# Kernel tuning notes

Hardware: AMD Instinct MI355X
Metric: run time of the kernel (lower is better)

Reference implementation:

```python
import jax, jax.numpy as jnp
import numpy as np

NUM_HEADS = 16

def setup_inputs() -> dict:
    key = jax.random.key(0)
    ks = jax.random.split(key, 7)
    B, Q, K, D = 4, 512, 4096, 1024
    return {
        'query':  jax.random.normal(ks[0], (B, Q, D), dtype=jnp.float32),
        'memory': jax.random.normal(ks[1], (B, K, D), dtype=jnp.float32),
        'bias':   jax.random.normal(ks[2], (B, K), dtype=jnp.float32),
        'Wq': jax.random.normal(ks[3], (D, D), dtype=jnp.float32) * (D ** -0.5),
        'Wk': jax.random.normal(ks[4], (D, D), dtype=jnp.float32) * (D ** -0.5),
        'Wv': jax.random.normal(ks[5], (D, D), dtype=jnp.float32) * (D ** -0.5),
        'Wo': jax.random.normal(ks[6], (D, D), dtype=jnp.float32) * (D ** -0.5),
    }

def reference(query, memory, bias, Wq, Wk, Wv, Wo):
    B, Qn, _ = query.shape
    _, Kn, _ = memory.shape
    H = NUM_HEADS
    E = Wq.shape[1]
    dh = E // H
    scale = dh ** -0.5
    # projections (bias-free linears), split heads: [B, H, len, dh]
    q = (query @ Wq).reshape(B, Qn, H, dh).transpose(0, 2, 1, 3)
    k = (memory @ Wk).reshape(B, Kn, H, dh).transpose(0, 2, 1, 3)
    v = (memory @ Wv).reshape(B, Kn, H, dh).transpose(0, 2, 1, 3)
    scores = jnp.einsum('bhqd,bhkd->bhqk', q, k) * scale
    scores = scores + bias[:, None, None, :]          # additive support bias over K
    weights = jax.nn.softmax(scores, axis=-1)          # dropout p=0.0 -> identity
    out = jnp.einsum('bhqk,bhkd->bhqd', weights, v)
    out = out.transpose(0, 2, 1, 3).reshape(B, Qn, E)
    return out @ Wo
```

## Files before the change

### kernel.cpp

```cpp
#include <hip/hip_runtime.h>

typedef __attribute__((ext_vector_type(8))) short bf16x8;
typedef __attribute__((ext_vector_type(4))) short bf16x4;
typedef __attribute__((ext_vector_type(4))) float f32x4;

#define MFMA32(a,b,c) __builtin_amdgcn_mfma_f32_16x16x32_bf16((a),(b),(c),0,0,0)
#define MFMA16(a,b,c) __builtin_amdgcn_mfma_f32_16x16x16bf16_1k((a),(b),(c),0,0,0)
#define LOG2E 1.44269504f

__device__ __forceinline__ unsigned short f2bf(float f) {
  unsigned int u = __float_as_uint(f);
  u += 0x7fffu + ((u >> 16) & 1u);
  return (unsigned short)(u >> 16);
}

__device__ __forceinline__ void cp16(const void* g, void* l) {
  __builtin_amdgcn_global_load_lds((const __attribute__((address_space(1))) void*)g,
                                   (__attribute__((address_space(3))) void*)l, 16, 0, 0);
}

__global__ void conv_both(const float* __restrict__ q, const float* __restrict__ m,
                          const float* __restrict__ bias,
                          unsigned short* __restrict__ qo, unsigned short* __restrict__ mo,
                          float* __restrict__ bz) {
  int i = blockIdx.x * 256 + threadIdx.x;
  if (i < 524288) {
    float4 v = ((const float4*)q)[i];
    ushort4 o; o.x = f2bf(v.x); o.y = f2bf(v.y); o.z = f2bf(v.z); o.w = f2bf(v.w);
    ((ushort4*)qo)[i] = o;
  } else if (i < 4718592) {
    int j = i - 524288;
    float4 v = ((const float4*)m)[j];
    ushort4 o; o.x = f2bf(v.x); o.y = f2bf(v.y); o.z = f2bf(v.z); o.w = f2bf(v.w);
    ((ushort4*)mo)[j] = o;
  } else {
    int j = i - 4718592;
    float4 v = ((const float4*)bias)[j];
    float4 o;
    o.x = __builtin_fmaf(v.x, LOG2E, -16.f);
    o.y = __builtin_fmaf(v.y, LOG2E, -16.f);
    o.z = __builtin_fmaf(v.z, LOG2E, -16.f);
    o.w = __builtin_fmaf(v.w, LOG2E, -16.f);
    ((float4*)bz)[j] = o;
  }
}

__global__ void transpose4(const float* __restrict__ Wq, const float* __restrict__ Wk,
                           const float* __restrict__ Wv, const float* __restrict__ Wo,
                           unsigned short* __restrict__ dst) {
  __shared__ float t[32][33];
  int z = blockIdx.z;
  const float* W = (z == 0) ? Wq : (z == 1) ? Wk : (z == 2) ? Wv : Wo;
  unsigned short* WT = dst + (size_t)z * 1048576;
  int bx = blockIdx.x * 32, by = blockIdx.y * 32;
  int x = threadIdx.x, y0 = threadIdx.y;
#pragma unroll
  for (int r = 0; r < 4; ++r)
    t[y0 + r * 8][x] = W[(size_t)(by + y0 + r * 8) * 1024 + bx + x];
  __syncthreads();
#pragma unroll
  for (int r = 0; r < 4; ++r)
    WT[(size_t)(bx + y0 + r * 8) * 1024 + by + x] = f2bf(t[x][y0 + r * 8]);
}

__global__ __launch_bounds__(256, 2) void gemm_kv(
    const unsigned short* __restrict__ A,
    const unsigned short* __restrict__ Bk,
    const unsigned short* __restrict__ Bv,
    unsigned short* __restrict__ Kp,
    unsigned short* __restrict__ Vt)
{
  __shared__ __attribute__((aligned(16))) unsigned short lds[16384];
  int w = threadIdx.x >> 6, lane = threadIdx.x & 63;
  int lh = lane & 15, q4 = lane >> 4;
  int id = blockIdx.x;
  int xcd = id & 7, j = id >> 3;
  int tm = (xcd * 16 + (j >> 3)) * 128;
  int tn = (j & 7) * 128;
  int wm = (w & 1) * 64, wn = (w >> 1) * 64;

  int srow = lane >> 2;
  int scol = ((lane & 3) ^ ((lane >> 3) & 3)) << 3;
  int q4s = (q4 ^ ((lh >> 1) & 3)) << 3;

  f32x4 acck[4][4] = {}, accv[4][4] = {};

  for (int k0 = 0; k0 < 1024; k0 += 32) {
#pragma unroll
    for (int i = 0; i < 2; ++i) {
      int c = w * 2 + i;
      int row = c * 16 + srow;
      cp16(A  + (size_t)(tm + row) * 1024 + k0 + scol, lds + c * 512);
      cp16(Bk + (size_t)(tn + row) * 1024 + k0 + scol, lds + 4096 + c * 512);
      cp16(Bv + (size_t)(tn + row) * 1024 + k0 + scol, lds + 8192 + c * 512);
    }
    __syncthreads();
    bf16x8 afr[4], bkf[4], bvf[4];
#pragma unroll
    for (int r = 0; r < 4; ++r)
      afr[r] = *(const bf16x8*)(lds + (wm + r * 16 + lh) * 32 + q4s);
#pragma unroll
    for (int c = 0; c < 4; ++c) {
      bkf[c] = *(const bf16x8*)(lds + 4096 + (wn + c * 16 + lh) * 32 + q4s);
      bvf[c] = *(const bf16x8*)(lds + 8192 + (wn + c * 16 + lh) * 32 + q4s);
    }
#pragma unroll
    for (int r = 0; r < 4; ++r)
#pragma unroll
      for (int c = 0; c < 4; ++c) {
        acck[r][c] = MFMA32(afr[r], bkf[c], acck[r][c]);
        accv[r][c] = MFMA32(afr[r], bvf[c], accv[r][c]);
      }
    __syncthreads();
  }

#pragma unroll
  for (int r = 0; r < 4; ++r)
#pragma unroll
    for (int c = 0; c < 4; ++c) {
      int row = tm + wm + r * 16 + q4 * 4;
      int col = tn + wn + c * 16 + lh;
#pragma unroll
      for (int e = 0; e < 4; ++e)
        Kp[(size_t)(row + e) * 1024 + col] = f2bf(acck[r][c][e]);
    }

#pragma unroll
  for (int r = 0; r < 4; ++r)
#pragma unroll
    for (int c = 0; c < 4; ++c) {
      int row = wm + r * 16 + q4 * 4;
      int col = wn + c * 16 + lh;
      ushort4 v4;
      v4.x = f2bf(accv[r][c][0]); v4.y = f2bf(accv[r][c][1]);
      v4.z = f2bf(accv[r][c][2]); v4.w = f2bf(accv[r][c][3]);
      *(ushort4*)(lds + col * 128 + (row ^ ((col & 15) << 3))) = v4;
    }
  __syncthreads();
#pragma unroll
  for (int pass = 0; pass < 8; ++pass) {
    int col = pass * 16 + (threadIdx.x >> 4);
    int jb = threadIdx.x & 15;
    const unsigned short* src = lds + col * 128 + ((jb ^ (col & 15)) << 3);
    *(int4*)(Vt + (size_t)(tn + col) * 16384 + tm + jb * 8) = *(const int4*)src;
  }
}

__global__ __launch_bounds__(256) void gemm_bt64(
    const unsigned short* __restrict__ A, const unsigned short* __restrict__ B,
    float* __restrict__ Cf, unsigned short* __restrict__ Cb,
    int M, int N, int K, float scale)
{
  __shared__ __attribute__((aligned(16))) unsigned short lds[6144];
  int w = threadIdx.x >> 6, lane = threadIdx.x & 63;
  int lh = lane & 15, q4 = lane >> 4;
  int tm = blockIdx.y * 128, tn = blockIdx.x * 64;
  int wm = (w & 1) * 64, wn = (w >> 1) * 32;

  int srow = lane >> 2;
  int scol = ((lane & 3) ^ ((lane >> 3) & 3)) << 3;
  int q4s = (q4 ^ ((lh >> 1) & 3)) << 3;

  f32x4 acc[4][2] = {};

  for (int k0 = 0; k0 < K; k0 += 32) {
#pragma unroll
    for (int i = 0; i < 2; ++i) {
      int c = w * 2 + i;
      int row = c * 16 + srow;
      cp16(A + (size_t)(tm + row) * K + k0 + scol, lds + c * 512);
    }
    {
      int row = w * 16 + srow;
      cp16(B + (size_t)(tn + row) * K + k0 + scol, lds + 4096 + w * 512);
    }
    __syncthreads();
    bf16x8 afr[4], bfr[2];
#pragma unroll
    for (int r = 0; r < 4; ++r)
      afr[r] = *(const bf16x8*)(lds + (wm + r * 16 + lh) * 32 + q4s);
#pragma unroll
    for (int c = 0; c < 2; ++c)
      bfr[c] = *(const bf16x8*)(lds + 4096 + (wn + c * 16 + lh) * 32 + q4s);
#pragma unroll
    for (int r = 0; r < 4; ++r)
#pragma unroll
      for (int c = 0; c < 2; ++c)
        acc[r][c] = MFMA32(afr[r], bfr[c], acc[r][c]);
    __syncthreads();
  }

#pragma unroll
  for (int r = 0; r < 4; ++r)
#pragma unroll
    for (int c = 0; c < 2; ++c)
#pragma unroll
      for (int e = 0; e < 4; ++e) {
        int row = tm + wm + r * 16 + q4 * 4 + e;
        int col = tn + wn + c * 16 + lh;
        if (Cb) Cb[(size_t)row * N + col] = f2bf(acc[r][c][e] * scale);
        else    Cf[(size_t)row * N + col] = acc[r][c][e] * scale;
      }
}

__global__ __launch_bounds__(256) void attn_kernel(
    const unsigned short* __restrict__ Q, const unsigned short* __restrict__ Kp,
    const unsigned short* __restrict__ VT, const float* __restrict__ bz,
    float* __restrict__ po, float* __restrict__ lp)
{
  __shared__ __attribute__((aligned(16))) unsigned short Klds[4096];
  __shared__ __attribute__((aligned(16))) unsigned short Vlds[4096];
  int w = threadIdx.x >> 6, lane = threadIdx.x & 63;
  int lh = lane & 15, q4 = lane >> 4;

  int id = blockIdx.x;
  int xcd = id & 7, j = id >> 3;
  int ql = j & 7;
  int half = ql & 1, qt = ql >> 1;
  int bh = (j >> 3) * 8 + xcd;
  int b = bh >> 4, h = bh & 15;
  int q0 = qt * 128;
  int t00 = half * 2048;

  const unsigned short* Qb = Q + (size_t)(b * 512 + q0 + w * 32) * 1024 + h * 64;
  const unsigned short* Kb = Kp + (size_t)(b * 4096) * 1024 + h * 64;
  const unsigned short* Vb = VT + (size_t)(h * 64) * 16384 + b * 4096;
  const float* bzg = bz + (size_t)b * 4096;

  bf16x8 bq[2][2];
#pragma unroll
  for (int s = 0; s < 2; ++s)
#pragma unroll
    for (int th = 0; th < 2; ++th)
      bq[s][th] = *(const bf16x8*)(Qb + (size_t)(s * 16 + lh) * 1024 + th * 32 + q4 * 8);

  f32x4 oa[2][4] = {};
  float ls[2] = {0.f, 0.f};

  int rl = lane >> 3, blk = lane & 7;
  int sw = ((blk ^ rl) * 8);

  for (int ti = 0; ti < 32; ++ti) {
    int t = t00 + ti * 64;
#pragma unroll
    for (int r = 0; r < 2; ++r) {
      int seg = r * 4 + w;
      int row = seg * 8 + rl;
      cp16(Kb + (size_t)(t + row) * 1024 + sw, Klds + seg * 512);
      cp16(Vb + (size_t)row * 16384 + t + sw, Vlds + seg * 512);
    }
    __syncthreads();

    float4 bz4[4];
#pragma unroll
    for (int c = 0; c < 4; ++c)
      bz4[c] = *(const float4*)(bzg + t + c * 16 + q4 * 4);

    bf16x8 kf[4][2];
#pragma unroll
    for (int c = 0; c < 4; ++c)
#pragma unroll
      for (int th = 0; th < 2; ++th)
        kf[c][th] = *(const bf16x8*)(Klds + (c * 16 + lh) * 64 + (((th << 2) + q4) ^ (lh & 7)) * 8);
    bf16x4 vf[4][4];
#pragma unroll
    for (int c = 0; c < 4; ++c)
#pragma unroll
      for (int c2 = 0; c2 < 4; ++c2)
        vf[c][c2] = *(const bf16x4*)(Vlds + (c2 * 16 + lh) * 64 +
                                     (((c << 1) + (q4 >> 1)) ^ (lh & 7)) * 8 + (q4 & 1) * 4);

#pragma unroll
    for (int s = 0; s < 2; ++s) {
#pragma unroll
      for (int c = 0; c < 4; ++c) {
        f32x4 z = {};
        z = MFMA32(kf[c][0], bq[s][0], z);
        z = MFMA32(kf[c][1], bq[s][1], z);
        float bzf[4] = {bz4[c].x, bz4[c].y, bz4[c].z, bz4[c].w};
        bf16x4 pb;
        float ps = 0.f;
#pragma unroll
        for (int e = 0; e < 4; ++e) {
          float p = __builtin_amdgcn_exp2f(z[e] + bzf[e]);
          ps += p;
          pb[e] = (short)f2bf(p);
        }
        ls[s] += ps;
#pragma unroll
        for (int c2 = 0; c2 < 4; ++c2)
          oa[s][c2] = MFMA16(vf[c][c2], pb, oa[s][c2]);
      }
    }
    __syncthreads();
  }

#pragma unroll
  for (int s = 0; s < 2; ++s) {
    ls[s] += __shfl_xor(ls[s], 16);
    ls[s] += __shfl_xor(ls[s], 32);
  }

  int sl = bh * 4 + qt;
  float* pslice = po + (size_t)(half * 256 + sl) * 8192;
#pragma unroll
  for (int s = 0; s < 2; ++s) {
    if (q4 == 0) lp[half * 32768 + sl * 128 + w * 32 + s * 16 + lh] = ls[s];
#pragma unroll
    for (int c2 = 0; c2 < 4; ++c2)
#pragma unroll
      for (int e = 0; e < 4; ++e)
        pslice[(c2 * 16 + q4 * 4 + e) * 128 + w * 32 + s * 16 + lh] = oa[s][c2][e];
  }
}

__global__ void norm_kernel(const float* __restrict__ po, const float* __restrict__ lp,
                            unsigned short* __restrict__ ao) {
  int g = blockIdx.x * 256 + threadIdx.x;
  int d8 = (g & 7) * 8;
  int rowid = g >> 3;
  int bh = rowid >> 9, rq = rowid & 511, qt = rq >> 7, qcol = rq & 127;
  int sl = bh * 4 + qt;
  const float* p0 = po + (size_t)sl * 8192;
  const float* p1 = po + (size_t)(256 + sl) * 8192;
  float l = lp[sl * 128 + qcol] + lp[32768 + sl * 128 + qcol];
  float inv = 1.f / l;
  unsigned short o8[8];
#pragma unroll
  for (int k = 0; k < 8; ++k)
    o8[k] = f2bf((p0[(d8 + k) * 128 + qcol] + p1[(d8 + k) * 128 + qcol]) * inv);
  int b = bh >> 4, h = bh & 15;
  unsigned short* dst = ao + (size_t)(b * 512 + qt * 128 + qcol) * 1024 + h * 64 + d8;
  *(ushort4*)dst = *(ushort4*)o8;
  *(ushort4*)(dst + 4) = *(ushort4*)(o8 + 4);
}

extern "C" void kernel_launch(void* const* d_in, const int* in_sizes, int n_in,
                              void* d_out, int out_size, void* d_ws, size_t ws_size,
                              hipStream_t stream) {
  const float* query  = (const float*)d_in[0];
  const float* memory = (const float*)d_in[1];
  const float* bias   = (const float*)d_in[2];
  const float* Wq     = (const float*)d_in[3];
  const float* Wk     = (const float*)d_in[4];
  const float* Wv     = (const float*)d_in[5];
  const float* Wo     = (const float*)d_in[6];
  float* out = (float*)d_out;

  unsigned short* ws  = (unsigned short*)d_ws;
  unsigned short* qbf = ws;
  unsigned short* mbf = qbf + 2097152;
  unsigned short* WqT = mbf + 16777216;
  unsigned short* WkT = WqT + 1048576;
  unsigned short* WvT = WkT + 1048576;
  unsigned short* WoT = WvT + 1048576;
  unsigned short* qp  = WoT + 1048576;
  unsigned short* kp  = qp + 2097152;
  unsigned short* vT  = kp + 16777216;
  unsigned short* ao  = vT + 16777216;
  float* bzw = (float*)(ao + 2097152);
  float* po = (float*)ws;
  float* lp = po + 4194304;

  conv_both<<<18448, 256, 0, stream>>>(query, memory, bias, qbf, mbf, bzw);
  transpose4<<<dim3(32, 32, 4), dim3(32, 8), 0, stream>>>(Wq, Wk, Wv, Wo, WqT);

  gemm_bt64<<<dim3(16, 16), 256, 0, stream>>>(qbf, WqT, nullptr, qp, 2048, 1024, 1024, 0.125f * LOG2E);
  gemm_kv<<<1024, 256, 0, stream>>>(mbf, WkT, WvT, kp, vT);

  attn_kernel<<<512, 256, 0, stream>>>(qp, kp, vT, bzw, po, lp);
  norm_kernel<<<1024, 256, 0, stream>>>(po, lp, ao);

  gemm_bt64<<<dim3(16, 16), 256, 0, stream>>>(ao, WoT, out, nullptr, 2048, 1024, 1024, 1.f);
}
```

Baseline: 303.0 us.

## Restructure KV projection GEMM with 256x128 tiles and double-buffered async pipeline

Rewrites the fused K/V projection GEMM to use 512-thread blocks on 256x128 output tiles with K-step 64, staging A/K/V tiles into a double-buffered 128KB LDS via direct global-to-LDS loads. The main loop is split into four MFMA phases with interleaved prefetches of the next tile, explicit vmcnt waits, raw s_barrier with sched barriers, and setprio around MFMA bursts. This aims to hide global load latency and raise MFMA utilisation. In exchange it uses much more LDS per block, which lowers occupancy, and relies on hand-tuned wait counts that must match the issue order exactly.

```diff
diff --git a/kernel.cpp b/kernel.cpp
--- a/kernel.cpp
+++ b/kernel.cpp
@@ -7,6 +7,10 @@
 #define MFMA32(a,b,c) __builtin_amdgcn_mfma_f32_16x16x32_bf16((a),(b),(c),0,0,0)
 #define MFMA16(a,b,c) __builtin_amdgcn_mfma_f32_16x16x16bf16_1k((a),(b),(c),0,0,0)
 #define LOG2E 1.44269504f
+
+#define BAR() do { asm volatile("s_barrier" ::: "memory"); \
+                   __builtin_amdgcn_sched_barrier(0); } while (0)
+#define VMW(n) asm volatile("s_waitcnt vmcnt(" #n ")" ::: "memory")
 
 __device__ __forceinline__ unsigned short f2bf(float f) {
   unsigned int u = __float_as_uint(f);
@@ -63,85 +67,145 @@
     WT[(size_t)(bx + y0 + r * 8) * 1024 + by + x] = f2bf(t[x][y0 + r * 8]);
 }
 
-__global__ __launch_bounds__(256, 2) void gemm_kv(
+__global__ __launch_bounds__(512, 2) void gemm_kv(
     const unsigned short* __restrict__ A,
     const unsigned short* __restrict__ Bk,
     const unsigned short* __restrict__ Bv,
     unsigned short* __restrict__ Kp,
     unsigned short* __restrict__ Vt)
 {
-  __shared__ __attribute__((aligned(16))) unsigned short lds[16384];
-  int w = threadIdx.x >> 6, lane = threadIdx.x & 63;
-  int lh = lane & 15, q4 = lane >> 4;
-  int id = blockIdx.x;
-  int xcd = id & 7, j = id >> 3;
-  int tm = (xcd * 16 + (j >> 3)) * 128;
-  int tn = (j & 7) * 128;
-  int wm = (w & 1) * 64, wn = (w >> 1) * 64;
-
-  int srow = lane >> 2;
-  int scol = ((lane & 3) ^ ((lane >> 3) & 3)) << 3;
-  int q4s = (q4 ^ ((lh >> 1) & 3)) << 3;
+  __shared__ __attribute__((aligned(16))) unsigned short lds[65536];
+  const int tid = threadIdx.x;
+  const int w = tid >> 6, lane = tid & 63;
+  const int lh = lane & 15, q4 = lane >> 4;
+  const int id = blockIdx.x;
+  const int xcd = id & 7, j = id >> 3;
+  const int tm = (xcd * 8 + (j >> 3)) * 256;
+  const int tn = (j & 7) * 128;
+  const int wm = (w >> 1) * 64, wn = (w & 1) * 64;
+
+  const int r8 = lane >> 3;
+  const int scol = ((lane & 7) ^ r8) * 8;
+  const int srow = w * 8 + r8;
+  const int fs0 = ((0 + q4) ^ (lh & 7)) * 8;
+  const int fs1 = ((4 + q4) ^ (lh & 7)) * 8;
+
+  const unsigned short* Ag = A  + (size_t)tm * 1024 + scol;
+  const unsigned short* Kg = Bk + (size_t)tn * 1024 + scol;
+  const unsigned short* Vg = Bv + (size_t)tn * 1024 + scol;
+
+#define STG_A(BUF,KT,I) cp16(Ag + (size_t)((I)*64 + srow) * 1024 + (KT)*64, \
+                             lds + (BUF)*32768 + (I)*4096 + w*512)
+#define STG_K(BUF,KT,I) cp16(Kg + (size_t)((I)*64 + srow) * 1024 + (KT)*64, \
+                             lds + (BUF)*32768 + 16384 + (I)*4096 + w*512)
+#define STG_V(BUF,KT,I) cp16(Vg + (size_t)((I)*64 + srow) * 1024 + (KT)*64, \
+                             lds + (BUF)*32768 + 24576 + (I)*4096 + w*512)
 
   f32x4 acck[4][4] = {}, accv[4][4] = {};
 
-  for (int k0 = 0; k0 < 1024; k0 += 32) {
-#pragma unroll
-    for (int i = 0; i < 2; ++i) {
-      int c = w * 2 + i;
-      int row = c * 16 + srow;
-      cp16(A  + (size_t)(tm + row) * 1024 + k0 + scol, lds + c * 512);
-      cp16(Bk + (size_t)(tn + row) * 1024 + k0 + scol, lds + 4096 + c * 512);
-      cp16(Bv + (size_t)(tn + row) * 1024 + k0 + scol, lds + 8192 + c * 512);
-    }
-    __syncthreads();
-    bf16x8 afr[4], bkf[4], bvf[4];
-#pragma unroll
-    for (int r = 0; r < 4; ++r)
-      afr[r] = *(const bf16x8*)(lds + (wm + r * 16 + lh) * 32 + q4s);
-#pragma unroll
-    for (int c = 0; c < 4; ++c) {
-      bkf[c] = *(const bf16x8*)(lds + 4096 + (wn + c * 16 + lh) * 32 + q4s);
-      bvf[c] = *(const bf16x8*)(lds + 8192 + (wn + c * 16 + lh) * 32 + q4s);
-    }
-#pragma unroll
-    for (int r = 0; r < 4; ++r)
-#pragma unroll
-      for (int c = 0; c < 4; ++c) {
-        acck[r][c] = MFMA32(afr[r], bkf[c], acck[r][c]);
-        accv[r][c] = MFMA32(afr[r], bvf[c], accv[r][c]);
-      }
-    __syncthreads();
-  }
-
-#pragma unroll
-  for (int r = 0; r < 4; ++r)
-#pragma unroll
-    for (int c = 0; c < 4; ++c) {
-      int row = tm + wm + r * 16 + q4 * 4;
-      int col = tn + wn + c * 16 + lh;
+  STG_A(0, 0, 0); STG_A(0, 0, 1); STG_A(0, 0, 2); STG_A(0, 0, 3);
+  STG_K(0, 0, 0); STG_K(0, 0, 1);
+  STG_V(0, 0, 0); STG_V(0, 0, 1);
+  STG_A(1, 1, 0); STG_A(1, 1, 1); STG_A(1, 1, 2); STG_A(1, 1, 3);
+  VMW(6);
+  BAR();
+
+#define KV_TILE(CURB, TP1, TP2, DO_SB, DO_SA, VM1N, DO_V3, VM3N)              \
+  {                                                                           \
+    const unsigned short* bse = lds + (CURB) * 32768;                         \
+    const int nx = (CURB) ^ 1;                                                \
+    bf16x8 a0[4], a1[4], bfr[4];                                              \
+                                                  \
+    _Pragma("unroll") for (int m = 0; m < 4; ++m)                             \
+      a0[m] = *(const bf16x8*)(bse + (wm + m * 16 + lh) * 64 + fs0);          \
+    _Pragma("unroll") for (int n = 0; n < 4; ++n)                             \
+      bfr[n] = *(const bf16x8*)(bse + 16384 + (wn + n * 16 + lh) * 64 + fs0); \
+    if (DO_SB) { STG_K(nx, TP1, 0); STG_K(nx, TP1, 1); }                      \
+    BAR();                                                                    \
+    __builtin_amdgcn_s_setprio(1);                                            \
+    _Pragma("unroll") for (int m = 0; m < 4; ++m)                             \
+      _Pragma("unroll") for (int n = 0; n < 4; ++n)                           \
+        acck[m][n] = MFMA32(a0[m], bfr[n], acck[m][n]);                       \
+    __builtin_amdgcn_s_setprio(0);                                            \
+    BAR();                                                                    \
+                                                  \
+    _Pragma("unroll") for (int m = 0; m < 4; ++m)                             \
+      a1[m] = *(const bf16x8*)(bse + (wm + m * 16 + lh) * 64 + fs1);          \
+    _Pragma("unroll") for (int n = 0; n < 4; ++n)                             \
+      bfr[n] = *(const bf16x8*)(bse + 16384 + (wn + n * 16 + lh) * 64 + fs1); \
+    if (DO_SB) { STG_V(nx, TP1, 0); STG_V(nx, TP1, 1); }                      \
+    BAR();                                                                    \
+    __builtin_amdgcn_s_setprio(1);                                            \
+    _Pragma("unroll") for (int m = 0; m < 4; ++m)                             \
+      _Pragma("unroll") for (int n = 0; n < 4; ++n)                           \
+        acck[m][n] = MFMA32(a1[m], bfr[n], acck[m][n]);                       \
+    __builtin_amdgcn_s_setprio(0);                                            \
+    VMW(VM1N);                                                                \
+    BAR();                                                                    \
+                                  \
+    _Pragma("unroll") for (int n = 0; n < 4; ++n)                             \
+      bfr[n] = *(const bf16x8*)(bse + 24576 + (wn + n * 16 + lh) * 64 + fs0); \
+    if (DO_SA) { STG_A(CURB, TP2, 0); STG_A(CURB, TP2, 1); }                  \
+    BAR();                                                                    \
+    __builtin_amdgcn_s_setprio(1);                                            \
+    _Pragma("unroll") for (int m = 0; m < 4; ++m)                             \
+      _Pragma("unroll") for (int n = 0; n < 4; ++n)                           \
+        accv[m][n] = MFMA32(a0[m], bfr[n], accv[m][n]);                       \
+    __builtin_amdgcn_s_setprio(0);                                            \
+    BAR();                                                                    \
+                                                  \
+    _Pragma("unroll") for (int n = 0; n < 4; ++n)                             \
+      bfr[n] = *(const bf16x8*)(bse + 24576 + (wn + n * 16 + lh) * 64 + fs1); \
+    if (DO_SA) { STG_A(CURB, TP2, 2); STG_A(CURB, TP2, 3); }                  \
+    BAR();                                                                    \
+    __builtin_amdgcn_s_setprio(1);                                            \
+    _Pragma("unroll") for (int m = 0; m < 4; ++m)                             \
+      _Pragma("unroll") for (int n = 0; n < 4; ++n)                           \
+        accv[m][n] = MFMA32(a1[m], bfr[n], accv[m][n]);                       \
+    __builtin_amdgcn_s_setprio(0);                                            \
+    if (DO_V3) { VMW(VM3N); }                                                 \
+    BAR();                                                                    \
+  }
+
+  for (int t = 0; t < 14; ++t) {
+    KV_TILE(t & 1, t + 1, t + 2, 1, 1, 8, 1, 6);
+  }
+  KV_TILE(0, 15, 16, 1, 0, 8, 1, 2);
+  KV_TILE(1, 16, 17, 0, 0, 0, 0, 0);
+
+#undef KV_TILE
+#undef STG_A
+#undef STG_K
+#undef STG_V
+
+#pragma unroll
+  for (int m = 0; m < 4; ++m)
+#pragma unroll
+    for (int n = 0; n < 4; ++n) {
+      int row = tm + wm + m * 16 + q4 * 4;
+      int col = tn + wn + n * 16 + lh;
 #pragma unroll
       for (int e = 0; e < 4; ++e)
-        Kp[(size_t)(row + e) * 1024 + col] = f2bf(acck[r][c][e]);
-    }
-
-#pragma unroll
-  for (int r = 0; r < 4; ++r)
-#pragma unroll
-    for (int c = 0; c < 4; ++c) {
-      int row = wm + r * 16 + q4 * 4;
-      int col = wn + c * 16 + lh;
+        Kp[(size_t)(row + e) * 1024 + col] = f2bf(acck[m][n][e]);
+    }
+
+#pragma unroll
+  for (int m = 0; m < 4; ++m)
+#pragma unroll
+    for (int n = 0; n < 4; ++n) {
+      int row = wm + m * 16 + q4 * 4;
+      int col = wn + n * 16 + lh;
       ushort4 v4;
-      v4.x = f2bf(accv[r][c][0]); v4.y = f2bf(accv[r][c][1]);
-      v4.z = f2bf(accv[r][c][2]); v4.w = f2bf(accv[r][c][3]);
-      *(ushort4*)(lds + col * 128 + (row ^ ((col & 15) << 3))) = v4;
+      v4.x = f2bf(accv[m][n][0]); v4.y = f2bf(accv[m][n][1]);
+      v4.z = f2bf(accv[m][n][2]); v4.w = f2bf(accv[m][n][3]);
+      *(ushort4*)(lds + col * 256 + (row ^ ((col & 31) << 3))) = v4;
     }
   __syncthreads();
 #pragma unroll
-  for (int pass = 0; pass < 8; ++pass) {
-    int col = pass * 16 + (threadIdx.x >> 4);
-    int jb = threadIdx.x & 15;
-    const unsigned short* src = lds + col * 128 + ((jb ^ (col & 15)) << 3);
+  for (int p = 0; p < 8; ++p) {
+    int col = p * 16 + (tid >> 5);
+    int jb = tid & 31;
+    const unsigned short* src = lds + col * 256 + ((jb ^ (col & 31)) << 3);
     *(int4*)(Vt + (size_t)(tn + col) * 16384 + tm + jb * 8) = *(const int4*)src;
   }
 }
@@ -366,7 +430,7 @@
   transpose4<<<dim3(32, 32, 4), dim3(32, 8), 0, stream>>>(Wq, Wk, Wv, Wo, WqT);
 
   gemm_bt64<<<dim3(16, 16), 256, 0, stream>>>(qbf, WqT, nullptr, qp, 2048, 1024, 1024, 0.125f * LOG2E);
-  gemm_kv<<<1024, 256, 0, stream>>>(mbf, WkT, WvT, kp, vT);
+  gemm_kv<<<512, 512, 0, stream>>>(mbf, WkT, WvT, kp, vT);
 
   attn_kernel<<<512, 256, 0, stream>>>(qp, kp, vT, bzw, po, lp);
   norm_kernel<<<1024, 256, 0, stream>>>(po, lp, ao);
```

After: 296.3 us. 2.2% less time.
